# Kernel optimization log

Measured on AMD Instinct MI355X. Metric: run time of the kernel, lower is better.

Reference implementation:

```python
import jax, jax.numpy as jnp
import numpy as np

B, S, D, H, DFF = 8, 1024, 1024, 16, 4096
DK = D // H
EPS = 1e-6
NEG = -1e9


def _layer_norm(x, gamma, beta):
    # Faithful to hand-rolled LN: torch std is unbiased (ddof=1), eps added to sigma.
    mu = jnp.mean(x, axis=-1, keepdims=True)
    sigma = jnp.std(x, axis=-1, keepdims=True, ddof=1)
    return gamma * (x - mu) / (EPS + sigma) + beta


def setup_inputs() -> dict:
    key = jax.random.key(0)
    ks = jax.random.split(key, 12)
    s = 0.02
    inp = {
        "x": jax.random.normal(ks[0], (B, S, D), dtype=jnp.float32),
        "src_mask": jnp.ones((B, 1, 1, S), dtype=jnp.int32),
        "Wq": jax.random.normal(ks[1], (D, D), dtype=jnp.float32) * s,
        "bq": jnp.zeros((D,), dtype=jnp.float32),
        "Wk": jax.random.normal(ks[2], (D, D), dtype=jnp.float32) * s,
        "bk": jnp.zeros((D,), dtype=jnp.float32),
        "Wv": jax.random.normal(ks[3], (D, D), dtype=jnp.float32) * s,
        "bv": jnp.zeros((D,), dtype=jnp.float32),
        "Wo": jax.random.normal(ks[4], (D, D), dtype=jnp.float32) * s,
        "bo": jnp.zeros((D,), dtype=jnp.float32),
        "W1": jax.random.normal(ks[5], (DFF, D), dtype=jnp.float32) * s,
        "b1": jnp.zeros((DFF,), dtype=jnp.float32),
        "W2": jax.random.normal(ks[6], (D, DFF), dtype=jnp.float32) * s,
        "b2": jnp.zeros((D,), dtype=jnp.float32),
        "g1": jnp.ones((1,), dtype=jnp.float32),
        "be1": jnp.zeros((1,), dtype=jnp.float32),
        "g2": jnp.ones((1,), dtype=jnp.float32),
        "be2": jnp.zeros((1,), dtype=jnp.float32),
    }
    return inp


def _encoder_block(x, src_mask, Wq, bq, Wk, bk, Wv, bv, Wo, bo,
                   W1, b1, W2, b2, g1, be1, g2, be2):
    # Multi-head self-attention (dropout = identity in eval)
    def split(h):  # [B,S,D] -> [B,H,S,DK]
        return h.reshape(B, S, H, DK).transpose(0, 2, 1, 3)

    q = split(x @ Wq.T + bq)
    k = split(x @ Wk.T + bk)
    v = split(x @ Wv.T + bv)

    scores = jnp.einsum("bhqd,bhkd->bhqk", q, k) / jnp.sqrt(jnp.float32(DK))
    scores = jnp.where(src_mask == 0, NEG, scores)
    probs = jax.nn.softmax(scores, axis=-1)
    attn = jnp.einsum("bhqk,bhkd->bhqd", probs, v)
    attn = attn.transpose(0, 2, 1, 3).reshape(B, S, D)
    attn = attn @ Wo.T + bo

    x1 = _layer_norm(x + attn, g1, be1)

    ff = jax.nn.relu(x1 @ W1.T + b1) @ W2.T + b2
    x2 = _layer_norm(x1 + ff, g2, be2)
    return x2


def reference(x, src_mask, Wq, bq, Wk, bk, Wv, bv, Wo, bo,
              W1, b1, W2, b2, g1, be1, g2, be2):
    return _encoder_block(x, src_mask, Wq, bq, Wk, bk, Wv, bv, Wo, bo,
                          W1, b1, W2, b2, g1, be1, g2, be2)
```

## Files before the change

### kernel.cpp

```cpp
#include <hip/hip_runtime.h>
#include <stdint.h>

#define BB 8
#define SS 1024
#define DD 1024
#define HH 16
#define DFF 4096
#define MT (BB*SS)

typedef __attribute__((ext_vector_type(8))) short bf16x8;
typedef __attribute__((ext_vector_type(4))) short s16x4;
typedef __attribute__((ext_vector_type(4))) float f32x4;
typedef __attribute__((ext_vector_type(16))) float f32x16;
typedef unsigned int u32x2 __attribute__((ext_vector_type(2)));

#define LOG2E 1.44269504088896340736f

__device__ __forceinline__ short f2bf(float f) {
  union { float f; uint32_t u; } v; v.f = f;
  uint32_t r = v.u + 0x7FFFu + ((v.u >> 16) & 1u);
  return (short)(r >> 16);
}
__device__ __forceinline__ float bf2f(short s) {
  union { uint32_t u; float f; } v; v.u = ((uint32_t)(uint16_t)s) << 16; return v.f;
}

__device__ __forceinline__ void gload_lds16(const void* g, void* l) {
  __builtin_amdgcn_global_load_lds(
      (__attribute__((address_space(1))) uint32_t*)(uintptr_t)g,
      (__attribute__((address_space(3))) uint32_t*)(uint32_t)(uintptr_t)l,
      16, 0, 0);
}

__device__ __forceinline__ uint32_t cvtpk(float lo, float hi) {
  uint32_t r;
  asm("v_cvt_pk_bf16_f32 %0, %1, %2" : "=v"(r) : "v"(lo), "v"(hi));
  return r;
}

__device__ __forceinline__ void swap2(uint32_t a, uint32_t b, uint32_t& x, uint32_t& y) {
#if __has_builtin(__builtin_amdgcn_permlane32_swap)
  u32x2 r = __builtin_amdgcn_permlane32_swap(a, b, false, false);
  x = r.x; y = r.y;
#else
  uint32_t asw = (uint32_t)__shfl_xor((int)a, 32, 64);
  uint32_t bsw = (uint32_t)__shfl_xor((int)b, 32, 64);
  bool h = (threadIdx.x & 32) != 0;
  x = h ? bsw : a;
  y = h ? b : asw;
#endif
}

__global__ __launch_bounds__(256) void cvt_bf16(const float* __restrict__ in,
                                                short* __restrict__ out, int n8) {
  int i = blockIdx.x * 256 + threadIdx.x;
  if (i >= n8) return;
  f32x4 a = *(const f32x4*)(in + (size_t)i * 8);
  f32x4 b = *(const f32x4*)(in + (size_t)i * 8 + 4);
  bf16x8 o;
  o[0]=f2bf(a[0]); o[1]=f2bf(a[1]); o[2]=f2bf(a[2]); o[3]=f2bf(a[3]);
  o[4]=f2bf(b[0]); o[5]=f2bf(b[1]); o[6]=f2bf(b[2]); o[7]=f2bf(b[3]);
  *(bf16x8*)(out + (size_t)i * 8) = o;
}

struct WCvt { const float* s[6]; short* d[6]; };
__global__ __launch_bounds__(256) void cvt_weights(WCvt w) {
  int u = blockIdx.x * 256 + threadIdx.x;
  if (u >= 1572864) return;
  int sel; int base;
  if      (u <  524288) { sel = u >> 17;            base = (u & 131071); }
  else if (u < 1048576) { sel = 4;                  base = u - 524288; }
  else                  { sel = 5;                  base = u - 1048576; }
  const float* in = w.s[sel] + (size_t)base * 8;
  short* out = w.d[sel] + (size_t)base * 8;
  f32x4 a = *(const f32x4*)(in);
  f32x4 b = *(const f32x4*)(in + 4);
  bf16x8 o;
  o[0]=f2bf(a[0]); o[1]=f2bf(a[1]); o[2]=f2bf(a[2]); o[3]=f2bf(a[3]);
  o[4]=f2bf(b[0]); o[5]=f2bf(b[1]); o[6]=f2bf(b[2]); o[7]=f2bf(b[3]);
  *(bf16x8*)(out) = o;
}

template<int BM, int RELU, int RES, int OUTF, int OUTB, int QKV, int SPLITK>
__global__ __launch_bounds__(512, 2) void gemm_ring(
    const short* __restrict__ A, const short* __restrict__ W,
    const float* __restrict__ bq, const float* __restrict__ bk,
    const float* __restrict__ bv, const float* __restrict__ res,
    float* __restrict__ outF, short* __restrict__ outB,
    int M, int N, int K, int Kc, float qscale)
{
  constexpr int AISS   = BM / 128;
  constexpr int SLOT_A = BM * 32 * 2;
  constexpr int SLOT   = SLOT_A + 256 * 32 * 2;
  constexpr int MI     = BM / 32;
  __shared__ __align__(16) char lds[3 * SLOT];

  const int tid = threadIdx.x, lane = tid & 63, wid = tid >> 6;
  const int wm = wid >> 2, wn = wid & 3;
  const int lrow = lane & 15, lk = lane >> 4;

  const int nwg = gridDim.x;
  const int cpx = nwg >> 3;
  const int id  = blockIdx.x;
  const int wg  = (id & 7) * cpx + (id >> 3);
  const int gx  = N >> 8;
  const int bx  = wg % gx, by = wg / gx;
  const int row0 = by * BM, col0 = bx * 256;
  const int koff = SPLITK ? blockIdx.z * Kc : 0;

  const int lineo = lane >> 3;
  const int rin   = lineo * 2 + ((lane >> 2) & 1);
  const int ksrc  = (lane & 3) ^ (lineo & 3);

  const short* Asrc[AISS];
#pragma unroll
  for (int j = 0; j < AISS; ++j)
    Asrc[j] = A + (size_t)(row0 + (wid * AISS + j) * 16 + rin) * K + koff + ksrc * 8;
  const short* Bsrc[2];
#pragma unroll
  for (int j = 0; j < 2; ++j)
    Bsrc[j] = W + (size_t)(col0 + (wid * 2 + j) * 16 + rin) * K + koff + ksrc * 8;

  const f32x4 z4 = {0.f, 0.f, 0.f, 0.f};
  f32x4 acc[MI][4];
#pragma unroll
  for (int i = 0; i < MI; ++i)
#pragma unroll
    for (int j = 0; j < 4; ++j) acc[i][j] = z4;

  const int NT = Kc >> 5;

  auto stage = [&](int ts, int s) {
    char* base = lds + s * SLOT;
    int ko = ts * 32;
#pragma unroll
    for (int j = 0; j < AISS; ++j)
      gload_lds16(Asrc[j] + ko, base + (wid * AISS + j) * 1024);
#pragma unroll
    for (int j = 0; j < 2; ++j)
      gload_lds16(Bsrc[j] + ko, base + SLOT_A + (wid * 2 + j) * 1024);
  };

  stage(0, 0);
  stage(1, 1);

  const int laneterm = (lrow >> 1) * 128 + (lrow & 1) * 64 + ((lk ^ ((lrow >> 1) & 3)) * 16);

  int sr = 0;
  for (int t = 0; t < NT; ++t) {
    const int sw = (sr == 0) ? 2 : sr - 1;
    const int ts = (t + 2 < NT) ? t + 2 : NT - 1;
    stage(ts, sw);
    if (AISS == 2) asm volatile("s_waitcnt vmcnt(8)" ::: "memory");
    else           asm volatile("s_waitcnt vmcnt(6)" ::: "memory");
    __builtin_amdgcn_s_barrier();
    __builtin_amdgcn_sched_barrier(0);

    const char* As = lds + sr * SLOT;
    const char* Bs = As + SLOT_A;
    bf16x8 af[MI], bfr[4];
#pragma unroll
    for (int mi = 0; mi < MI; ++mi)
      af[mi] = *(const bf16x8*)(As + wm * (BM * 32) + mi * 1024 + laneterm);
#pragma unroll
    for (int ni = 0; ni < 4; ++ni)
      bfr[ni] = *(const bf16x8*)(Bs + wn * 4096 + ni * 1024 + laneterm);

    __builtin_amdgcn_s_setprio(1);
#pragma unroll
    for (int mi = 0; mi < MI; ++mi)
#pragma unroll
      for (int ni = 0; ni < 4; ++ni)
        acc[mi][ni] = __builtin_amdgcn_mfma_f32_16x16x32_bf16(af[mi], bfr[ni], acc[mi][ni], 0, 0, 0);
    __builtin_amdgcn_s_setprio(0);

    __builtin_amdgcn_s_barrier();
    sr = (sr == 2) ? 0 : sr + 1;
  }

  const int sel    = QKV ? (col0 >> 10) : 0;
  const float* bias = QKV ? (sel == 0 ? bq : (sel == 1 ? bk : bv)) : bq;
  const int strideN = QKV ? 1024 : N;
  short* outBp = OUTB ? (outB + (QKV ? (size_t)sel * MT * DD : 0)
                              + (SPLITK ? (size_t)blockIdx.z * M * strideN : 0)) : outB;
  const float scl = (QKV && sel == 0) ? qscale : 1.f;

#pragma unroll
  for (int mi = 0; mi < MI; ++mi) {
#pragma unroll
    for (int ni = 0; ni < 4; ++ni) {
      int col  = col0 + wn * 64 + ni * 16 + lrow;
      int coll = QKV ? (col & 1023) : col;
      float bvv = SPLITK ? 0.f : bias[coll];
#pragma unroll
      for (int r = 0; r < 4; ++r) {
        int row = row0 + wm * (BM / 2) + mi * 16 + lk * 4 + r;
        float v = acc[mi][ni][r] + bvv;
        if (QKV) v *= scl;
        if (RELU) v = fmaxf(v, 0.f);
        size_t idx = (size_t)row * strideN + coll;
        if (RES)  v += res[idx];
        if (OUTF) outF[idx] = v;
        if (OUTB) outBp[idx] = f2bf(v);
      }
    }
  }
}

__global__ __launch_bounds__(256) void transpose_v(const short* __restrict__ Vb,
                                                   short* __restrict__ Vt) {
  const int s = blockIdx.x * 256 + threadIdx.x;
  const int u = blockIdx.y;
  const int bh = blockIdx.z, b = bh >> 4, h = bh & 15;
  bf16x8 v = *(const bf16x8*)(Vb + ((size_t)(b * SS + s)) * DD + h * 64 + u * 8);
  size_t ob = ((size_t)bh * 64 + u * 8) * SS + s;
#pragma unroll
  for (int j = 0; j < 8; ++j) Vt[ob + (size_t)j * SS] = v[j];
}

__global__ __launch_bounds__(256) void attn_flash3(
    const short* __restrict__ Qm, const short* __restrict__ Km,
    const short* __restrict__ Vtg, const int* __restrict__ mask,
    short* __restrict__ Om)
{
  __shared__ short KsB[2 * 64 * 64];
  __shared__ short VsB[2 * 64 * 64];
  __shared__ float ma_all[SS];
  __shared__ float fb[4 * 32];

  const int tid = threadIdx.x, lane = tid & 63, wid = tid >> 6;
  const int l31 = lane & 31, hi = lane >> 5;
  const int bh = blockIdx.y, b = bh >> 4, h = bh & 15;
  const int q0 = blockIdx.x * 128 + wid * 32;

  {
    const int* mrow = mask + b * SS;
#pragma unroll
    for (int i = 0; i < 4; ++i) {
      int idx = i * 256 + tid;
      ma_all[idx] = (mrow[idx] == 0) ? -1.442695e9f : 0.f;
    }
  }

  bf16x8 qf[4];
  {
    const short* qrow = Qm + ((size_t)(b * SS + q0 + l31)) * DD + h * 64;
#pragma unroll
    for (int t = 0; t < 4; ++t) qf[t] = *(const bf16x8*)(qrow + t * 16 + hi * 8);
  }

  f32x16 acc0, acc1;
#pragma unroll
  for (int i = 0; i < 16; ++i) { acc0[i] = 0.f; acc1[i] = 0.f; }
  float m_r = -3e38f, l_r = 0.f;

  const int srow = tid >> 3;
  const int su = tid & 7;

  auto stageKV = [&](int kt2, int bi) {
#pragma unroll
    for (int i = 0; i < 2; ++i) {
      int r = i * 32 + srow;
      int uu = su ^ (r & 7);
      gload_lds16(Km + ((size_t)(b * SS + kt2 + r)) * DD + h * 64 + uu * 8,
                  KsB + bi * 4096 + (i * 256 + wid * 64) * 8);
      gload_lds16(Vtg + ((size_t)(bh * 64 + r)) * SS + kt2 + uu * 8,
                  VsB + bi * 4096 + (i * 256 + wid * 64) * 8);
    }
  };

  __syncthreads();
  stageKV(0, 0);

  for (int t = 0; t < 16; ++t) {
    if (t < 15) {
      stageKV((t + 1) << 6, (t + 1) & 1);
      asm volatile("s_waitcnt vmcnt(4)" ::: "memory");
    } else {
      asm volatile("s_waitcnt vmcnt(0)" ::: "memory");
    }
    __builtin_amdgcn_s_barrier();
    __builtin_amdgcn_sched_barrier(0);

    const short* Ks = KsB + (t & 1) * 4096;
    const short* Vs = VsB + (t & 1) * 4096;

    f32x16 s0, s1;
#pragma unroll
    for (int i = 0; i < 16; ++i) { s0[i] = 0.f; s1[i] = 0.f; }
#pragma unroll
    for (int t4 = 0; t4 < 4; ++t4) {
      int u = (t4 * 2 + hi) ^ (l31 & 7);
      bf16x8 k0 = *(const bf16x8*)(Ks + l31 * 64 + u * 8);
      bf16x8 k1 = *(const bf16x8*)(Ks + (32 + l31) * 64 + u * 8);
      s0 = __builtin_amdgcn_mfma_f32_32x32x16_bf16(k0, qf[t4], s0, 0, 0, 0);
      s1 = __builtin_amdgcn_mfma_f32_32x32x16_bf16(k1, qf[t4], s1, 0, 0, 0);
    }

    const float* map = ma_all + (t << 6);
    float p0[16], p1[16];
    float mx = -3e38f;
#pragma unroll
    for (int g = 0; g < 4; ++g) {
      f32x4 a0 = *(const f32x4*)(map + g * 8 + hi * 4);
      f32x4 a1 = *(const f32x4*)(map + 32 + g * 8 + hi * 4);
#pragma unroll
      for (int j = 0; j < 4; ++j) {
        float v0 = s0[g * 4 + j] + a0[j];
        float v1 = s1[g * 4 + j] + a1[j];
        p0[g * 4 + j] = v0; p1[g * 4 + j] = v1;
        mx = fmaxf(mx, fmaxf(v0, v1));
      }
    }
    mx = fmaxf(mx, __shfl_xor(mx, 32, 64));

    if (!__all(mx <= m_r + 8.f)) {
      float mn  = fmaxf(m_r, mx);
      float fac = exp2f(m_r - mn);
      m_r = mn;
      l_r *= fac;
      fb[wid * 32 + l31] = fac;
#pragma unroll
      for (int g = 0; g < 4; ++g) {
        f32x4 fv = *(const f32x4*)(fb + wid * 32 + g * 8 + hi * 4);
#pragma unroll
        for (int j = 0; j < 4; ++j) { acc0[g * 4 + j] *= fv[j]; acc1[g * 4 + j] *= fv[j]; }
      }
    }

    float rs = 0.f;
#pragma unroll
    for (int r = 0; r < 16; ++r) {
      p0[r] = exp2f(p0[r] - m_r);
      p1[r] = exp2f(p1[r] - m_r);
      rs += p0[r] + p1[r];
    }
    rs += __shfl_xor(rs, 32, 64);
    l_r += rs;

    uint32_t w0[8], w1[8];
#pragma unroll
    for (int m = 0; m < 8; ++m) {
      w0[m] = cvtpk(p0[2 * m], p0[2 * m + 1]);
      w1[m] = cvtpk(p1[2 * m], p1[2 * m + 1]);
    }
    uint32_t pa[4][4];
    swap2(w0[0], w0[2], pa[0][0], pa[0][2]);
    swap2(w0[1], w0[3], pa[0][1], pa[0][3]);
    swap2(w0[4], w0[6], pa[1][0], pa[1][2]);
    swap2(w0[5], w0[7], pa[1][1], pa[1][3]);
    swap2(w1[0], w1[2], pa[2][0], pa[2][2]);
    swap2(w1[1], w1[3], pa[2][1], pa[2][3]);
    swap2(w1[4], w1[6], pa[3][0], pa[3][2]);
    swap2(w1[5], w1[7], pa[3][1], pa[3][3]);

#pragma unroll
    for (int kc = 0; kc < 4; ++kc) {
      union { uint32_t w[4]; bf16x8 v; } pu;
      pu.w[0] = pa[kc][0]; pu.w[1] = pa[kc][1]; pu.w[2] = pa[kc][2]; pu.w[3] = pa[kc][3];
      int u = (kc * 2 + hi) ^ (l31 & 7);
      bf16x8 v0 = *(const bf16x8*)(Vs + l31 * 64 + u * 8);
      bf16x8 v1 = *(const bf16x8*)(Vs + (32 + l31) * 64 + u * 8);
      acc0 = __builtin_amdgcn_mfma_f32_32x32x16_bf16(pu.v, v0, acc0, 0, 0, 0);
      acc1 = __builtin_amdgcn_mfma_f32_32x32x16_bf16(pu.v, v1, acc1, 0, 0, 0);
    }

    __builtin_amdgcn_s_barrier();
  }

  fb[wid * 32 + l31] = 1.f / l_r;
#pragma unroll
  for (int g = 0; g < 4; ++g) {
    f32x4 rv = *(const f32x4*)(fb + wid * 32 + g * 8 + hi * 4);
#pragma unroll
    for (int j = 0; j < 4; ++j) {
      int q = q0 + g * 8 + hi * 4 + j;
      size_t base = ((size_t)(b * SS + q)) * DD + h * 64 + l31;
      Om[base]      = f2bf(acc0[g * 4 + j] * rv[j]);
      Om[base + 32] = f2bf(acc1[g * 4 + j] * rv[j]);
    }
  }
}

template<int WRITE_BF16>
__global__ __launch_bounds__(256) void layernorm_k(
    float* __restrict__ x, short* __restrict__ xb,
    const float* __restrict__ g, const float* __restrict__ be)
{
  const int row = blockIdx.x, tid = threadIdx.x;
  float* xr = x + (size_t)row * DD;
  f32x4 a = *(const f32x4*)(xr + tid * 4);
  float s  = a[0] + a[1] + a[2] + a[3];
  float ss = a[0]*a[0] + a[1]*a[1] + a[2]*a[2] + a[3]*a[3];
#pragma unroll
  for (int o = 1; o < 64; o <<= 1) { s += __shfl_xor(s, o, 64); ss += __shfl_xor(ss, o, 64); }
  __shared__ float red[8];
  const int wid = tid >> 6, lane = tid & 63;
  if (lane == 0) { red[wid] = s; red[4 + wid] = ss; }
  __syncthreads();
  s  = red[0] + red[1] + red[2] + red[3];
  ss = red[4] + red[5] + red[6] + red[7];
  float mu  = s * (1.f / DD);
  float var = fmaxf((ss - (float)DD * mu * mu) * (1.f / (DD - 1)), 0.f);
  float inv = g[0] / (1e-6f + sqrtf(var));
  float bb  = be[0];
#pragma unroll
  for (int j = 0; j < 4; ++j) a[j] = (a[j] - mu) * inv + bb;
  *(f32x4*)(xr + tid * 4) = a;
  if (WRITE_BF16) {
    s16x4 o;
#pragma unroll
    for (int j = 0; j < 4; ++j) o[j] = f2bf(a[j]);
    *(s16x4*)(xb + (size_t)row * DD + tid * 4) = o;
  }
}

__global__ __launch_bounds__(256) void ln2_combine(
    const short* __restrict__ P0, const short* __restrict__ P1,
    const float* __restrict__ x1, const float* __restrict__ b2,
    const float* __restrict__ g, const float* __restrict__ be,
    float* __restrict__ out)
{
  const int row = blockIdx.x, tid = threadIdx.x;
  s16x4 pa = *(const s16x4*)(P0 + (size_t)row * DD + tid * 4);
  s16x4 pb = *(const s16x4*)(P1 + (size_t)row * DD + tid * 4);
  f32x4 xr = *(const f32x4*)(x1 + (size_t)row * DD + tid * 4);
  f32x4 bb4 = *(const f32x4*)(b2 + tid * 4);
  f32x4 a;
#pragma unroll
  for (int j = 0; j < 4; ++j) a[j] = bf2f(pa[j]) + bf2f(pb[j]) + bb4[j] + xr[j];
  float s  = a[0] + a[1] + a[2] + a[3];
  float ss = a[0]*a[0] + a[1]*a[1] + a[2]*a[2] + a[3]*a[3];
#pragma unroll
  for (int o = 1; o < 64; o <<= 1) { s += __shfl_xor(s, o, 64); ss += __shfl_xor(ss, o, 64); }
  __shared__ float red[8];
  const int wid = tid >> 6, lane = tid & 63;
  if (lane == 0) { red[wid] = s; red[4 + wid] = ss; }
  __syncthreads();
  s  = red[0] + red[1] + red[2] + red[3];
  ss = red[4] + red[5] + red[6] + red[7];
  float mu  = s * (1.f / DD);
  float var = fmaxf((ss - (float)DD * mu * mu) * (1.f / (DD - 1)), 0.f);
  float inv = g[0] / (1e-6f + sqrtf(var));
  float bb  = be[0];
#pragma unroll
  for (int j = 0; j < 4; ++j) a[j] = (a[j] - mu) * inv + bb;
  *(f32x4*)(out + (size_t)row * DD + tid * 4) = a;
}

extern "C" void kernel_launch(void* const* d_in, const int* in_sizes, int n_in,
                              void* d_out, int out_size, void* d_ws, size_t ws_size,
                              hipStream_t stream) {
  const float* x    = (const float*)d_in[0];
  const int*   mask = (const int*)d_in[1];
  const float* Wq = (const float*)d_in[2];  const float* bq = (const float*)d_in[3];
  const float* Wk = (const float*)d_in[4];  const float* bk = (const float*)d_in[5];
  const float* Wv = (const float*)d_in[6];  const float* bv = (const float*)d_in[7];
  const float* Wo = (const float*)d_in[8];  const float* bo = (const float*)d_in[9];
  const float* W1 = (const float*)d_in[10]; const float* b1 = (const float*)d_in[11];
  const float* W2 = (const float*)d_in[12]; const float* b2 = (const float*)d_in[13];
  const float* g1 = (const float*)d_in[14]; const float* be1 = (const float*)d_in[15];
  const float* g2 = (const float*)d_in[16]; const float* be2 = (const float*)d_in[17];
  float* out = (float*)d_out;

  char* ws = (char*)d_ws;
  size_t off = 0;
  auto alloc = [&](size_t bytes) -> char* {
    char* p = ws + off; off += (bytes + 255) & ~(size_t)255; return p;
  };
  short* xb  = (short*)alloc((size_t)MT * DD * 2);
  short* wqb = (short*)alloc((size_t)DD * DD * 2);
  short* wkb = (short*)alloc((size_t)DD * DD * 2);
  short* wvb = (short*)alloc((size_t)DD * DD * 2);
  short* wob = (short*)alloc((size_t)DD * DD * 2);
  short* w1b = (short*)alloc((size_t)DFF * DD * 2);
  short* w2b = (short*)alloc((size_t)DD * DFF * 2);
  short* Qb  = (short*)alloc((size_t)MT * DD * 2);
  short* Kb  = (short*)alloc((size_t)MT * DD * 2);
  short* Vb  = (short*)alloc((size_t)MT * DD * 2);
  short* Ab  = (short*)alloc((size_t)MT * DD * 2);
  float* x1  = (float*)alloc((size_t)MT * DD * 4);
  short* F1  = Qb;
  short* x1b = xb;
  short* Vt  = (short*)x1;
  short* P01 = (short*)ws;
  (void)wkb; (void)wvb; (void)Kb; (void)Vb;

  const float qscale = 0.125f * LOG2E;

  cvt_bf16<<<(MT * DD / 8 + 255) / 256, 256, 0, stream>>>(x, xb, MT * DD / 8);
  WCvt wc;
  wc.s[0] = Wq; wc.s[1] = Wk; wc.s[2] = Wv; wc.s[3] = Wo; wc.s[4] = W1; wc.s[5] = W2;
  wc.d[0] = wqb; wc.d[1] = wkb; wc.d[2] = wvb; wc.d[3] = wob; wc.d[4] = w1b; wc.d[5] = w2b;
  cvt_weights<<<(1572864 + 255) / 256, 256, 0, stream>>>(wc);

  gemm_ring<256,0,0,0,1,1,0><<<dim3((3072/256)*(MT/256)), 512, 0, stream>>>(
      xb, wqb, bq, bk, bv, nullptr, nullptr, Qb, MT, 3072, DD, DD, qscale);

  transpose_v<<<dim3(SS/256, 8, BB*HH), 256, 0, stream>>>(Vb, Vt);
  attn_flash3<<<dim3(SS/128, BB*HH), 256, 0, stream>>>(Qb, Kb, Vt, mask, Ab);

  gemm_ring<128,0,1,1,0,0,0><<<dim3((DD/256)*(MT/128)), 512, 0, stream>>>(
      Ab, wob, bo, bo, bo, x, x1, nullptr, MT, DD, DD, DD, 1.f);
  layernorm_k<1><<<MT, 256, 0, stream>>>(x1, x1b, g1, be1);

  gemm_ring<256,1,0,0,1,0,0><<<dim3((DFF/256)*(MT/256)), 512, 0, stream>>>(
      x1b, w1b, b1, b1, b1, nullptr, nullptr, F1, MT, DFF, DD, DD, 1.f);

  gemm_ring<256,0,0,0,1,0,1><<<dim3((DD/256)*(MT/256), 1, 2), 512, 0, stream>>>(
      F1, w2b, b2, b2, b2, nullptr, nullptr, P01, MT, DD, DFF, DFF/2, 1.f);
  ln2_combine<<<MT, 256, 0, stream>>>(P01, P01 + (size_t)MT * DD, x1, b2, g2, be2, out);
}
```

Measured before the change: 375.0 us.

## Add double-buffered BK=64 GEMM kernel with interleaved LDS reads for 256-row GEMMs

Introduces gemm_8p, a 256x256-tile GEMM that stages 64-wide K chunks into a double-buffered 128KB LDS with an XOR swizzle. It splits each K-step into four sub-phases that load A fragments and then issue MFMAs, with barriers between them. The new kernel replaces the triple-ring kernel for the QKV, FFN1 and split-K FFN2 GEMMs, aiming to halve the number of outer K iterations and barrier overhead. The attention kernel also raises wave priority around its MFMA blocks. The larger LDS footprint may cap occupancy at one block per CU despite launch_bounds(512,2), and the extra in-loop barriers may add stalls.

```diff
diff --git a/kernel.cpp b/kernel.cpp
--- a/kernel.cpp
+++ b/kernel.cpp
@@ -81,13 +81,137 @@
   *(bf16x8*)(out) = o;
 }
 
-template<int BM, int RELU, int RES, int OUTF, int OUTB, int QKV, int SPLITK>
+template<int RELU, int QKV, int SPLITK>
+__global__ __launch_bounds__(512, 2) void gemm_8p(
+    const short* __restrict__ A, const short* __restrict__ W,
+    const float* __restrict__ bq, const float* __restrict__ bk,
+    const float* __restrict__ bv, short* __restrict__ outB,
+    int M, int N, int K, int Kc, float qscale)
+{
+  __shared__ __align__(16) char lds[131072];
+  const int tid = threadIdx.x, lane = tid & 63, wid = tid >> 6;
+  const int wm = wid >> 2, wn = wid & 3;
+  const int lrow = lane & 15, lk = lane >> 4;
+
+  const int nwg = gridDim.x, cpx = nwg >> 3, id = blockIdx.x;
+  const int wg = (id & 7) * cpx + (id >> 3);
+  const int gx = N >> 8;
+  const int bx = wg % gx, by = wg / gx;
+  const int row0 = by * 256, col0 = bx * 256;
+  const int koff = SPLITK ? blockIdx.z * Kc : 0;
+
+  const int sr8  = lane >> 3;
+  const int ksrc = ((lane & 7) ^ sr8) * 8;
+  const short* Ag[4]; const short* Bg[4];
+#pragma unroll
+  for (int c = 0; c < 4; ++c) {
+    int r = (c >> 1) * 128 + wid * 16 + (c & 1) * 8 + sr8;
+    Ag[c] = A + (size_t)(row0 + r) * K + koff + ksrc;
+    Bg[c] = W + (size_t)(col0 + r) * K + koff + ksrc;
+  }
+
+  auto stage = [&](int ts, int nb) {
+    char* base = lds + nb * 65536;
+    const int ko = ts * 64;
+#pragma unroll
+    for (int c = 0; c < 4; ++c)
+      gload_lds16(Ag[c] + ko, base + (c >> 1) * 16384 + (wid * 2 + (c & 1)) * 1024);
+#pragma unroll
+    for (int c = 0; c < 4; ++c)
+      gload_lds16(Bg[c] + ko, base + 32768 + (c >> 1) * 16384 + (wid * 2 + (c & 1)) * 1024);
+  };
+
+  const f32x4 z4 = {0.f, 0.f, 0.f, 0.f};
+  f32x4 acc[8][4];
+#pragma unroll
+  for (int i = 0; i < 8; ++i)
+#pragma unroll
+    for (int j = 0; j < 4; ++j) acc[i][j] = z4;
+
+  const int NT = Kc >> 6;
+  stage(0, 0);
+
+  const int x0   = ((lk ^ (lrow & 7)) * 16);
+  const int arow = wm * 128 + lrow;
+  const int brow = wn * 64 + lrow;
+
+  for (int T = 0; T < NT; ++T) {
+    const int buf = T & 1;
+    const char* Ab = lds + buf * 65536;
+    const char* Bb = Ab + 32768;
+
+    const int ts = (T + 1 < NT) ? T + 1 : NT - 1;
+    stage(ts, buf ^ 1);
+    asm volatile("s_waitcnt vmcnt(8)" ::: "memory");
+    __builtin_amdgcn_s_barrier();
+    __builtin_amdgcn_sched_barrier(0);
+
+    bf16x8 bfr[4][2];
+#pragma unroll
+    for (int ni = 0; ni < 4; ++ni) {
+      const char* p = Bb + (brow + ni * 16) * 128;
+      bfr[ni][0] = *(const bf16x8*)(p + x0);
+      bfr[ni][1] = *(const bf16x8*)(p + (x0 ^ 64));
+    }
+
+#pragma unroll
+    for (int q = 0; q < 4; ++q) {
+      const char* p0 = Ab + (arow + (2 * q) * 16) * 128;
+      const char* p1 = Ab + (arow + (2 * q + 1) * 16) * 128;
+      bf16x8 a00 = *(const bf16x8*)(p0 + x0);
+      bf16x8 a01 = *(const bf16x8*)(p0 + (x0 ^ 64));
+      bf16x8 a10 = *(const bf16x8*)(p1 + x0);
+      bf16x8 a11 = *(const bf16x8*)(p1 + (x0 ^ 64));
+      asm volatile("s_waitcnt lgkmcnt(0)" ::: "memory");
+      __builtin_amdgcn_sched_barrier(0);
+      __builtin_amdgcn_s_setprio(1);
+#pragma unroll
+      for (int ni = 0; ni < 4; ++ni) {
+        acc[2*q][ni]   = __builtin_amdgcn_mfma_f32_16x16x32_bf16(a00, bfr[ni][0], acc[2*q][ni],   0, 0, 0);
+        acc[2*q][ni]   = __builtin_amdgcn_mfma_f32_16x16x32_bf16(a01, bfr[ni][1], acc[2*q][ni],   0, 0, 0);
+        acc[2*q+1][ni] = __builtin_amdgcn_mfma_f32_16x16x32_bf16(a10, bfr[ni][0], acc[2*q+1][ni], 0, 0, 0);
+        acc[2*q+1][ni] = __builtin_amdgcn_mfma_f32_16x16x32_bf16(a11, bfr[ni][1], acc[2*q+1][ni], 0, 0, 0);
+      }
+      __builtin_amdgcn_s_setprio(0);
+      __builtin_amdgcn_s_barrier();
+    }
+  }
+
+  asm volatile("s_waitcnt vmcnt(0)" ::: "memory");
+
+  const int sel    = QKV ? (col0 >> 10) : 0;
+  const float* bias = QKV ? (sel == 0 ? bq : (sel == 1 ? bk : bv)) : bq;
+  const int strideN = QKV ? 1024 : N;
+  short* outBp = outB + (QKV ? (size_t)sel * MT * DD : 0)
+                      + (SPLITK ? (size_t)blockIdx.z * M * strideN : 0);
+  const float scl = (QKV && sel == 0) ? qscale : 1.f;
+
+#pragma unroll
+  for (int mi = 0; mi < 8; ++mi) {
+#pragma unroll
+    for (int ni = 0; ni < 4; ++ni) {
+      int col  = col0 + wn * 64 + ni * 16 + lrow;
+      int coll = QKV ? (col & 1023) : col;
+      float bvv = SPLITK ? 0.f : bias[coll];
+#pragma unroll
+      for (int r = 0; r < 4; ++r) {
+        int row = row0 + wm * 128 + mi * 16 + lk * 4 + r;
+        float v = acc[mi][ni][r] + bvv;
+        if (QKV) v *= scl;
+        if (RELU) v = fmaxf(v, 0.f);
+        outBp[(size_t)row * strideN + coll] = f2bf(v);
+      }
+    }
+  }
+}
+
+template<int BM, int RELU, int RES, int OUTF, int OUTB, int QKV>
 __global__ __launch_bounds__(512, 2) void gemm_ring(
     const short* __restrict__ A, const short* __restrict__ W,
     const float* __restrict__ bq, const float* __restrict__ bk,
     const float* __restrict__ bv, const float* __restrict__ res,
     float* __restrict__ outF, short* __restrict__ outB,
-    int M, int N, int K, int Kc, float qscale)
+    int M, int N, int K, float qscale)
 {
   constexpr int AISS   = BM / 128;
   constexpr int SLOT_A = BM * 32 * 2;
@@ -106,7 +230,6 @@
   const int gx  = N >> 8;
   const int bx  = wg % gx, by = wg / gx;
   const int row0 = by * BM, col0 = bx * 256;
-  const int koff = SPLITK ? blockIdx.z * Kc : 0;
 
   const int lineo = lane >> 3;
   const int rin   = lineo * 2 + ((lane >> 2) & 1);
@@ -115,11 +238,11 @@
   const short* Asrc[AISS];
 #pragma unroll
   for (int j = 0; j < AISS; ++j)
-    Asrc[j] = A + (size_t)(row0 + (wid * AISS + j) * 16 + rin) * K + koff + ksrc * 8;
+    Asrc[j] = A + (size_t)(row0 + (wid * AISS + j) * 16 + rin) * K + ksrc * 8;
   const short* Bsrc[2];
 #pragma unroll
   for (int j = 0; j < 2; ++j)
-    Bsrc[j] = W + (size_t)(col0 + (wid * 2 + j) * 16 + rin) * K + koff + ksrc * 8;
+    Bsrc[j] = W + (size_t)(col0 + (wid * 2 + j) * 16 + rin) * K + ksrc * 8;
 
   const f32x4 z4 = {0.f, 0.f, 0.f, 0.f};
   f32x4 acc[MI][4];
@@ -128,7 +251,7 @@
 #pragma unroll
     for (int j = 0; j < 4; ++j) acc[i][j] = z4;
 
-  const int NT = Kc >> 5;
+  const int NT = K >> 5;
 
   auto stage = [&](int ts, int s) {
     char* base = lds + s * SLOT;
@@ -151,8 +274,8 @@
     const int sw = (sr == 0) ? 2 : sr - 1;
     const int ts = (t + 2 < NT) ? t + 2 : NT - 1;
     stage(ts, sw);
-    if (AISS == 2) asm volatile("s_waitcnt vmcnt(8)" ::: "memory");
-    else           asm volatile("s_waitcnt vmcnt(6)" ::: "memory");
+    if constexpr (AISS == 2) asm volatile("s_waitcnt vmcnt(8)" ::: "memory");
+    else                     asm volatile("s_waitcnt vmcnt(6)" ::: "memory");
     __builtin_amdgcn_s_barrier();
     __builtin_amdgcn_sched_barrier(0);
 
@@ -178,30 +301,22 @@
     sr = (sr == 2) ? 0 : sr + 1;
   }
 
-  const int sel    = QKV ? (col0 >> 10) : 0;
-  const float* bias = QKV ? (sel == 0 ? bq : (sel == 1 ? bk : bv)) : bq;
-  const int strideN = QKV ? 1024 : N;
-  short* outBp = OUTB ? (outB + (QKV ? (size_t)sel * MT * DD : 0)
-                              + (SPLITK ? (size_t)blockIdx.z * M * strideN : 0)) : outB;
-  const float scl = (QKV && sel == 0) ? qscale : 1.f;
-
+  const float* bias = bq;
 #pragma unroll
   for (int mi = 0; mi < MI; ++mi) {
 #pragma unroll
     for (int ni = 0; ni < 4; ++ni) {
       int col  = col0 + wn * 64 + ni * 16 + lrow;
-      int coll = QKV ? (col & 1023) : col;
-      float bvv = SPLITK ? 0.f : bias[coll];
+      float bvv = bias[col];
 #pragma unroll
       for (int r = 0; r < 4; ++r) {
         int row = row0 + wm * (BM / 2) + mi * 16 + lk * 4 + r;
         float v = acc[mi][ni][r] + bvv;
-        if (QKV) v *= scl;
         if (RELU) v = fmaxf(v, 0.f);
-        size_t idx = (size_t)row * strideN + coll;
+        size_t idx = (size_t)row * N + col;
         if (RES)  v += res[idx];
         if (OUTF) outF[idx] = v;
-        if (OUTB) outBp[idx] = f2bf(v);
+        if (OUTB) outB[idx] = f2bf(v);
       }
     }
   }
@@ -288,6 +403,7 @@
     f32x16 s0, s1;
 #pragma unroll
     for (int i = 0; i < 16; ++i) { s0[i] = 0.f; s1[i] = 0.f; }
+    __builtin_amdgcn_s_setprio(1);
 #pragma unroll
     for (int t4 = 0; t4 < 4; ++t4) {
       int u = (t4 * 2 + hi) ^ (l31 & 7);
@@ -296,6 +412,7 @@
       s0 = __builtin_amdgcn_mfma_f32_32x32x16_bf16(k0, qf[t4], s0, 0, 0, 0);
       s1 = __builtin_amdgcn_mfma_f32_32x32x16_bf16(k1, qf[t4], s1, 0, 0, 0);
     }
+    __builtin_amdgcn_s_setprio(0);
 
     const float* map = ma_all + (t << 6);
     float p0[16], p1[16];
@@ -354,6 +471,7 @@
     swap2(w1[4], w1[6], pa[3][0], pa[3][2]);
     swap2(w1[5], w1[7], pa[3][1], pa[3][3]);
 
+    __builtin_amdgcn_s_setprio(1);
 #pragma unroll
     for (int kc = 0; kc < 4; ++kc) {
       union { uint32_t w[4]; bf16x8 v; } pu;
@@ -364,6 +482,7 @@
       acc0 = __builtin_amdgcn_mfma_f32_32x32x16_bf16(pu.v, v0, acc0, 0, 0, 0);
       acc1 = __builtin_amdgcn_mfma_f32_32x32x16_bf16(pu.v, v1, acc1, 0, 0, 0);
     }
+    __builtin_amdgcn_s_setprio(0);
 
     __builtin_amdgcn_s_barrier();
   }
@@ -494,20 +613,20 @@
   wc.d[0] = wqb; wc.d[1] = wkb; wc.d[2] = wvb; wc.d[3] = wob; wc.d[4] = w1b; wc.d[5] = w2b;
   cvt_weights<<<(1572864 + 255) / 256, 256, 0, stream>>>(wc);
 
-  gemm_ring<256,0,0,0,1,1,0><<<dim3((3072/256)*(MT/256)), 512, 0, stream>>>(
-      xb, wqb, bq, bk, bv, nullptr, nullptr, Qb, MT, 3072, DD, DD, qscale);
+  gemm_8p<0,1,0><<<dim3((3072/256)*(MT/256)), 512, 0, stream>>>(
+      xb, wqb, bq, bk, bv, Qb, MT, 3072, DD, DD, qscale);
 
   transpose_v<<<dim3(SS/256, 8, BB*HH), 256, 0, stream>>>(Vb, Vt);
   attn_flash3<<<dim3(SS/128, BB*HH), 256, 0, stream>>>(Qb, Kb, Vt, mask, Ab);
 
-  gemm_ring<128,0,1,1,0,0,0><<<dim3((DD/256)*(MT/128)), 512, 0, stream>>>(
-      Ab, wob, bo, bo, bo, x, x1, nullptr, MT, DD, DD, DD, 1.f);
+  gemm_ring<128,0,1,1,0,0><<<dim3((DD/256)*(MT/128)), 512, 0, stream>>>(
+      Ab, wob, bo, bo, bo, x, x1, nullptr, MT, DD, DD, 1.f);
   layernorm_k<1><<<MT, 256, 0, stream>>>(x1, x1b, g1, be1);
 
-  gemm_ring<256,1,0,0,1,0,0><<<dim3((DFF/256)*(MT/256)), 512, 0, stream>>>(
-      x1b, w1b, b1, b1, b1, nullptr, nullptr, F1, MT, DFF, DD, DD, 1.f);
-
-  gemm_ring<256,0,0,0,1,0,1><<<dim3((DD/256)*(MT/256), 1, 2), 512, 0, stream>>>(
-      F1, w2b, b2, b2, b2, nullptr, nullptr, P01, MT, DD, DFF, DFF/2, 1.f);
+  gemm_8p<1,0,0><<<dim3((DFF/256)*(MT/256)), 512, 0, stream>>>(
+      x1b, w1b, b1, b1, b1, F1, MT, DFF, DD, DD, 1.f);
+
+  gemm_8p<0,0,1><<<dim3((DD/256)*(MT/256), 1, 2), 512, 0, stream>>>(
+      F1, w2b, b2, b2, b2, P01, MT, DD, DFF, DFF/2, 1.f);
   ln2_combine<<<MT, 256, 0, stream>>>(P01, P01 + (size_t)MT * DD, x1, b2, g2, be2, out);
 }
```

New measurement: 371.3 us. About the same (-1.0%).
